# Performance work log

Measured on AMD Instinct MI355X. Metric: run time of the kernel, lower is better.

## Reference

```python
import jax, jax.numpy as jnp
import numpy as np

NUM_HEADS = 8

def setup_inputs() -> dict:
    key = jax.random.key(0)
    ks = jax.random.split(key, 7)
    B, Cin, H, W = 4, 256, 56, 56
    Cout = 256
    s = 1.0 / np.sqrt(Cin)
    return {
        "x": jax.random.normal(ks[0], (B, Cin, H, W), dtype=jnp.float32),
        "wq": jax.random.normal(ks[1], (Cout, Cin), dtype=jnp.float32) * s,
        "bq": jax.random.normal(ks[2], (Cout,), dtype=jnp.float32) * s,
        "wk": jax.random.normal(ks[3], (Cout, Cin), dtype=jnp.float32) * s,
        "bk": jax.random.normal(ks[4], (Cout,), dtype=jnp.float32) * s,
        "wv": jax.random.normal(ks[5], (Cout, Cin), dtype=jnp.float32) * s,
        "bv": jax.random.normal(ks[6], (Cout,), dtype=jnp.float32) * s,
    }

def _proj(x, w, b):
    # 1x1 conv == per-pixel linear: [B,Cin,H,W] x [Cout,Cin] -> [B,Cout,H,W]
    return jnp.einsum('bchw,oc->bohw', x, w) + b[None, :, None, None]

def reference(x, wq, bq, wk, bk, wv, bv):
    B, _, H, W = x.shape
    Cout = wq.shape[0]
    hd = Cout // NUM_HEADS
    N = H * W
    # project and reshape to [B, heads, N, head_dim]
    def split_heads(t):
        return t.reshape(B, NUM_HEADS, hd, N).transpose(0, 1, 3, 2)
    q = split_heads(_proj(x, wq, bq))
    k = split_heads(_proj(x, wk, bk))
    v = split_heads(_proj(x, wv, bv))
    scores = jnp.einsum('bhnd,bhmd->bhnm', q, k) / jnp.sqrt(jnp.float32(hd))
    attn = jax.nn.softmax(scores, axis=-1)          # [B, heads, N, N]
    out = jnp.einsum('bhnm,bhmd->bhnd', attn, v)    # [B, heads, N, hd]
    out = out.transpose(0, 1, 3, 2).reshape(B, Cout, H, W)
    return out
```

## Files before the change

kernel.cpp:

```cpp
#include <hip/hip_runtime.h>
#include <math.h>


#define NB   4
#define CIN  256
#define NPIX 3136
#define NH   8
#define HD   32
#define QSC  0.25503837897544295f

typedef float          f32x4  __attribute__((ext_vector_type(4)));
typedef short          bf16x8 __attribute__((ext_vector_type(8)));
typedef unsigned int   u32x4  __attribute__((ext_vector_type(4)));
typedef unsigned int   u32x2  __attribute__((ext_vector_type(2)));
typedef unsigned short u16x4  __attribute__((ext_vector_type(4)));

static __device__ __forceinline__ unsigned short f2bf(float f) {
  union { float f; unsigned u; } v; v.f = f;
  return (unsigned short)((v.u + 0x7fffu + ((v.u >> 16) & 1u)) >> 16);
}

static __device__ __forceinline__ float fast_exp2(float x) {
#if __has_builtin(__builtin_amdgcn_exp2f)
  return __builtin_amdgcn_exp2f(x);
#else
  return exp2f(x);
#endif
}

static __device__ __forceinline__ unsigned cvt_pk_bf16(float lo, float hi) {
  unsigned r;
  asm("v_cvt_pk_bf16_f32 %0, %1, %2" : "=v"(r) : "v"(lo), "v"(hi));
  return r;
}

static __device__ __forceinline__ void gload_lds16(const void* g, void* l) {
  __builtin_amdgcn_global_load_lds(
      (__attribute__((address_space(1))) const void*)g,
      (__attribute__((address_space(3))) void*)l, 16, 0, 0);
}

static __device__ __forceinline__ bf16x8 lds_frag16(const unsigned char* p) {
  u32x4 u = *(const u32x4*)p;
  return __builtin_bit_cast(bf16x8, u);
}

__global__ __launch_bounds__(256) void k_xpose(const float* __restrict__ x,
                                               unsigned short* __restrict__ xbT) {
  __shared__ unsigned short tile[64][66];
  const int n0 = blockIdx.x * 64, c0 = blockIdx.y * 64, b = blockIdx.z;
  const int t = threadIdx.x;
  const int cl = t >> 4, nl = (t & 15) * 4;
#pragma unroll
  for (int rep = 0; rep < 4; ++rep) {
    const int c = cl + rep * 16;
    f32x4 v = *(const f32x4*)(x + ((size_t)(b * CIN + c0 + c)) * NPIX + n0 + nl);
    tile[nl + 0][c] = f2bf(v.x);
    tile[nl + 1][c] = f2bf(v.y);
    tile[nl + 2][c] = f2bf(v.z);
    tile[nl + 3][c] = f2bf(v.w);
  }
  __syncthreads();
  const int nr = t >> 2, co = (t & 3) * 16;
  unsigned pw[8];
#pragma unroll
  for (int j = 0; j < 8; ++j)
    pw[j] = (unsigned)tile[nr][co + 2 * j] | ((unsigned)tile[nr][co + 2 * j + 1] << 16);
  unsigned short* dst = xbT + ((size_t)(b * NPIX + n0 + nr)) * 256 + c0 + co;
  u32x4 lo = {pw[0], pw[1], pw[2], pw[3]};
  u32x4 hi = {pw[4], pw[5], pw[6], pw[7]};
  *(u32x4*)dst = lo;
  *(u32x4*)(dst + 8) = hi;
}

__global__ __launch_bounds__(256) void k_wconv(const float* __restrict__ wq,
                                               const float* __restrict__ wk,
                                               const float* __restrict__ wv,
                                               unsigned short* __restrict__ wb) {
  const int i = blockIdx.x * 256 + threadIdx.x;
  const int mat = i >> 16, idx = i & 65535;
  const float* w = (mat == 0) ? wq : (mat == 1 ? wk : wv);
  const float s = (mat == 0) ? QSC : 1.0f;
  wb[i] = f2bf(w[idx] * s);
}

__global__ __launch_bounds__(256) void k_proj(
    const unsigned short* __restrict__ xbT, const unsigned short* __restrict__ wb,
    const float* __restrict__ bq, const float* __restrict__ bk,
    const float* __restrict__ bv,
    unsigned short* __restrict__ qws, unsigned short* __restrict__ kws,
    unsigned short* __restrict__ vtws) {
  __shared__ alignas(16) unsigned char lds[20480];
  const int b = blockIdx.y & 3, mat = blockIdx.y >> 2;
  const int n0 = blockIdx.x * 64;
  const int t = threadIdx.x, l = t & 63, wid = t >> 6, g = l >> 4, q = l & 15;
  const unsigned short* wmat = wb + mat * (256 * 256);

  f32x4 acc[4][4] = {};

  for (int ks = 0; ks < 8; ++ks) {
#pragma unroll
    for (int r = 0; r < 4; ++r) {
      const unsigned short* src = wmat + ((wid + 4 * r) * 16 + q) * 256 + ks * 32 + g * 8;
      gload_lds16(src, lds + (r * 256 + t) * 16);
    }
    gload_lds16(xbT + ((size_t)(b * NPIX + n0 + wid * 16 + q)) * 256 + ks * 32 + g * 8,
                lds + 16384 + t * 16);
    __syncthreads();

    bf16x8 wa[4], xf[4];
#pragma unroll
    for (int r = 0; r < 4; ++r) wa[r] = lds_frag16(lds + (r * 256 + wid * 64 + l) * 16);
#pragma unroll
    for (int nt = 0; nt < 4; ++nt) xf[nt] = lds_frag16(lds + 16384 + (nt * 64 + l) * 16);
#pragma unroll
    for (int r = 0; r < 4; ++r)
#pragma unroll
      for (int nt = 0; nt < 4; ++nt)
        acc[r][nt] = __builtin_amdgcn_mfma_f32_16x16x32_bf16(wa[r], xf[nt], acc[r][nt], 0, 0, 0);
    __syncthreads();
  }

  const float* bias = (mat == 0) ? bq : (mat == 1 ? bk : bv);
  const float bsc = (mat == 0) ? QSC : 1.0f;
#pragma unroll
  for (int r = 0; r < 4; ++r) {
    const int ob = (wid + 4 * r) * 16 + g * 4;
    const int h = ob >> 5, d0 = ob & 31;
    const float b0 = bias[ob + 0] * bsc, b1 = bias[ob + 1] * bsc;
    const float b2 = bias[ob + 2] * bsc, b3 = bias[ob + 3] * bsc;
#pragma unroll
    for (int nt = 0; nt < 4; ++nt) {
      const int n = n0 + nt * 16 + q;
      f32x4 a = acc[r][nt];
      if (mat < 2) {
        unsigned short* dst = (mat == 0) ? qws : kws;
        u16x4 pk = {f2bf(a.x + b0), f2bf(a.y + b1), f2bf(a.z + b2), f2bf(a.w + b3)};
        *(u16x4*)(dst + ((size_t)((b * NH + h) * NPIX + n)) * HD + d0) = pk;
      } else {
        unsigned short* vr = vtws + ((size_t)((b * NH + h) * HD + d0)) * NPIX + n;
        vr[0] = f2bf(a.x + b0);
        vr[(size_t)NPIX] = f2bf(a.y + b1);
        vr[(size_t)2 * NPIX] = f2bf(a.z + b2);
        vr[(size_t)3 * NPIX] = f2bf(a.w + b3);
      }
    }
  }
}

__global__ __launch_bounds__(256) void k_attn(
    const unsigned short* __restrict__ qws, const unsigned short* __restrict__ kws,
    const unsigned short* __restrict__ vtws, float* __restrict__ out) {
  __shared__ alignas(16) unsigned char lds[32768];
  const int bid = blockIdx.x;
  const int xcd = bid & 7, inner = bid >> 3;
  const int qt = inner % 25;
  const int bh = 8 * (inner / 25) + xcd;
  const int q0 = qt * 128;
  const int t = threadIdx.x, l = t & 63, wid = t >> 6, g = l >> 4, q = l & 15;

  const int nA = q0 + wid * 32 + q;
  const int nB = nA + 16;
  const int rowA = (nA < NPIX) ? nA : (NPIX - 1);
  const int rowB = (nB < NPIX) ? nB : (NPIX - 1);

  u32x4 quA = *(const u32x4*)(qws + ((size_t)(bh * NPIX + rowA)) * HD + g * 8);
  u32x4 quB = *(const u32x4*)(qws + ((size_t)(bh * NPIX + rowB)) * HD + g * 8);
  const bf16x8 qfA = __builtin_bit_cast(bf16x8, quA);
  const bf16x8 qfB = __builtin_bit_cast(bf16x8, quB);
  const u32x4 onesu = {0x3F803F80u, 0x3F803F80u, 0x3F803F80u, 0x3F803F80u};
  const bf16x8 onesf = __builtin_bit_cast(bf16x8, onesu);
  const f32x4 zero4 = {0.f, 0.f, 0.f, 0.f};

  f32x4 oA0 = zero4, oA1 = zero4, oB0 = zero4, oB1 = zero4;
  f32x4 sumA = zero4, sumB = zero4;

  const unsigned short* ksrc = kws + ((size_t)(bh * NPIX + wid * 16 + q)) * HD + g * 8;
  const unsigned short* vsrc =
      vtws + ((size_t)(bh * HD + (wid >> 1) * 16 + q)) * NPIX + (wid & 1) * 32 + g * 8;

  unsigned char* const pbaseA = lds + 16384 + wid * 4096;
  unsigned char* const pbaseB = pbaseA + 2048;

  unsigned bofs = 0;
  gload_lds16(ksrc, lds + t * 16);
  gload_lds16(vsrc, lds + 4096 + t * 16);
  __syncthreads();

  for (int kt = 0; kt < 49; ++kt) {
    if (kt < 48) {
      gload_lds16(ksrc + (size_t)(kt + 1) * 64 * HD, lds + (bofs ^ 8192) + t * 16);
      gload_lds16(vsrc + (kt + 1) * 64, lds + (bofs ^ 8192) + 4096 + t * 16);
    }
    const unsigned char* kb = lds + bofs;
    const unsigned char* vb = lds + bofs + 4096;

    f32x4 sA[4], sB[4];
    __builtin_amdgcn_s_setprio(1);
#pragma unroll
    for (int jj = 0; jj < 4; ++jj) {
      bf16x8 kf = lds_frag16(kb + (jj * 64 + l) * 16);
      sA[jj] = __builtin_amdgcn_mfma_f32_16x16x32_bf16(kf, qfA, zero4, 0, 0, 0);
      sB[jj] = __builtin_amdgcn_mfma_f32_16x16x32_bf16(kf, qfB, zero4, 0, 0, 0);
    }
    __builtin_amdgcn_s_setprio(0);

    {
      unsigned pw[8];
#pragma unroll
      for (int jj = 0; jj < 4; ++jj) {
#pragma unroll
        for (int rp = 0; rp < 2; ++rp) {
          float p0 = fast_exp2(sA[jj][2 * rp + 0]);
          float p1 = fast_exp2(sA[jj][2 * rp + 1]);
          pw[jj * 2 + rp] = cvt_pk_bf16(p0, p1);
        }
      }
      u32x4 c0 = {pw[0], pw[1], pw[2], pw[3]};
      u32x4 c1 = {pw[4], pw[5], pw[6], pw[7]};
      *(u32x4*)(pbaseA + l * 16) = c0;
      *(u32x4*)(pbaseA + 1024 + l * 16) = c1;
    }
    {
      unsigned pw[8];
#pragma unroll
      for (int jj = 0; jj < 4; ++jj) {
#pragma unroll
        for (int rp = 0; rp < 2; ++rp) {
          float p0 = fast_exp2(sB[jj][2 * rp + 0]);
          float p1 = fast_exp2(sB[jj][2 * rp + 1]);
          pw[jj * 2 + rp] = cvt_pk_bf16(p0, p1);
        }
      }
      u32x4 c0 = {pw[0], pw[1], pw[2], pw[3]};
      u32x4 c1 = {pw[4], pw[5], pw[6], pw[7]};
      *(u32x4*)(pbaseB + l * 16) = c0;
      *(u32x4*)(pbaseB + 1024 + l * 16) = c1;
    }

    asm volatile("s_waitcnt lgkmcnt(0)" ::: "memory");
    __builtin_amdgcn_sched_barrier(0);

#pragma unroll
    for (int c = 0; c < 2; ++c) {
      bf16x8 v0 = lds_frag16(vb + (c * 64 + l) * 16);
      bf16x8 v1 = lds_frag16(vb + (128 + c * 64 + l) * 16);

      const unsigned char* pA = pbaseA + c * 1024 + q * 16 + (g & 2) * 4;
      u32x2 alo = *(const u32x2*)(pA + ((2 * g) & 3) * 256);
      u32x2 ahi = *(const u32x2*)(pA + ((2 * g + 1) & 3) * 256);
      u32x4 au = {alo.x, alo.y, ahi.x, ahi.y};
      bf16x8 pfA = __builtin_bit_cast(bf16x8, au);

      const unsigned char* pB = pbaseB + c * 1024 + q * 16 + (g & 2) * 4;
      u32x2 blo = *(const u32x2*)(pB + ((2 * g) & 3) * 256);
      u32x2 bhi = *(const u32x2*)(pB + ((2 * g + 1) & 3) * 256);
      u32x4 bu = {blo.x, blo.y, bhi.x, bhi.y};
      bf16x8 pfB = __builtin_bit_cast(bf16x8, bu);

      __builtin_amdgcn_s_setprio(1);
      oA0 = __builtin_amdgcn_mfma_f32_16x16x32_bf16(v0, pfA, oA0, 0, 0, 0);
      oA1 = __builtin_amdgcn_mfma_f32_16x16x32_bf16(v1, pfA, oA1, 0, 0, 0);
      sumA = __builtin_amdgcn_mfma_f32_16x16x32_bf16(onesf, pfA, sumA, 0, 0, 0);
      oB0 = __builtin_amdgcn_mfma_f32_16x16x32_bf16(v0, pfB, oB0, 0, 0, 0);
      oB1 = __builtin_amdgcn_mfma_f32_16x16x32_bf16(v1, pfB, oB1, 0, 0, 0);
      sumB = __builtin_amdgcn_mfma_f32_16x16x32_bf16(onesf, pfB, sumB, 0, 0, 0);
      __builtin_amdgcn_s_setprio(0);
    }

    __syncthreads();
    bofs ^= 8192;
  }

  if (nA < NPIX) {
    const float inv = 1.0f / sumA[0];
    float* ob = out + (size_t)(bh * HD) * NPIX + nA;
#pragma unroll
    for (int r = 0; r < 4; ++r) {
      ob[(size_t)(g * 4 + r) * NPIX] = oA0[r] * inv;
      ob[(size_t)(16 + g * 4 + r) * NPIX] = oA1[r] * inv;
    }
  }
  if (nB < NPIX) {
    const float inv = 1.0f / sumB[0];
    float* ob = out + (size_t)(bh * HD) * NPIX + nB;
#pragma unroll
    for (int r = 0; r < 4; ++r) {
      ob[(size_t)(g * 4 + r) * NPIX] = oB0[r] * inv;
      ob[(size_t)(16 + g * 4 + r) * NPIX] = oB1[r] * inv;
    }
  }
}

extern "C" void kernel_launch(void* const* d_in, const int* in_sizes, int n_in,
                              void* d_out, int out_size, void* d_ws, size_t ws_size,
                              hipStream_t stream) {
  const float* x  = (const float*)d_in[0];
  const float* wq = (const float*)d_in[1];
  const float* bq = (const float*)d_in[2];
  const float* wk = (const float*)d_in[3];
  const float* bk = (const float*)d_in[4];
  const float* wv = (const float*)d_in[5];
  const float* bv = (const float*)d_in[6];
  float* out = (float*)d_out;

  unsigned char* ws = (unsigned char*)d_ws;
  unsigned short* xbT  = (unsigned short*)(ws);
  unsigned short* wb   = (unsigned short*)(ws + 6422528);
  unsigned short* qws  = (unsigned short*)(ws + 6815744);
  unsigned short* kws  = (unsigned short*)(ws + 13238272);
  unsigned short* vtws = (unsigned short*)(ws + 19660800);

  k_xpose<<<dim3(49, 4, 4), 256, 0, stream>>>(x, xbT);
  k_wconv<<<dim3(768), 256, 0, stream>>>(wq, wk, wv, wb);
  k_proj<<<dim3(49, 12), 256, 0, stream>>>(xbT, wb, bq, bk, bv, qws, kws, vtws);
  k_attn<<<dim3(800), 256, 0, stream>>>(qws, kws, vtws, out);
}
```

Measured before the change: 115.5 us.

## Software-pipeline attention loop: PV of previous tile overlaps QK of current tile

Restructures the attention main loop so each iteration runs the P·V MFMAs for the previous key tile and then the QK^T plus exp for the current tile. The K/V staging buffers go from double to triple buffering and the P buffer is double buffered, which removes the in-loop lgkmcnt wait and sched barrier between computing P and consuming it. LDS use grows from 32KB to 56KB per block, which may lower occupancy, and the loop gains an extra iteration for prologue and epilogue.

```diff
diff --git a/kernel.cpp b/kernel.cpp
--- a/kernel.cpp
+++ b/kernel.cpp
@@ -151,7 +151,7 @@
 __global__ __launch_bounds__(256) void k_attn(
     const unsigned short* __restrict__ qws, const unsigned short* __restrict__ kws,
     const unsigned short* __restrict__ vtws, float* __restrict__ out) {
-  __shared__ alignas(16) unsigned char lds[32768];
+  __shared__ alignas(16) unsigned char lds[57344];
   const int bid = blockIdx.x;
   const int xcd = bid & 7, inner = bid >> 3;
   const int qt = inner % 25;
@@ -179,98 +179,101 @@
   const unsigned short* vsrc =
       vtws + ((size_t)(bh * HD + (wid >> 1) * 16 + q)) * NPIX + (wid & 1) * 32 + g * 8;
 
-  unsigned char* const pbaseA = lds + 16384 + wid * 4096;
-  unsigned char* const pbaseB = pbaseA + 2048;
-
-  unsigned bofs = 0;
-  gload_lds16(ksrc, lds + t * 16);
-  gload_lds16(vsrc, lds + 4096 + t * 16);
+#define STG(kt_, s_)                                                          \
+  do {                                                                        \
+    gload_lds16(ksrc + (size_t)(kt_) * 64 * HD, lds + (s_) * 8192 + t * 16);  \
+    gload_lds16(vsrc + (size_t)(kt_) * 64, lds + (s_) * 8192 + 4096 + t * 16);\
+  } while (0)
+
+  STG(0, 0);
   __syncthreads();
 
-  for (int kt = 0; kt < 49; ++kt) {
-    if (kt < 48) {
-      gload_lds16(ksrc + (size_t)(kt + 1) * 64 * HD, lds + (bofs ^ 8192) + t * 16);
-      gload_lds16(vsrc + (kt + 1) * 64, lds + (bofs ^ 8192) + 4096 + t * 16);
-    }
-    const unsigned char* kb = lds + bofs;
-    const unsigned char* vb = lds + bofs + 4096;
-
-    f32x4 sA[4], sB[4];
-    __builtin_amdgcn_s_setprio(1);
-#pragma unroll
-    for (int jj = 0; jj < 4; ++jj) {
-      bf16x8 kf = lds_frag16(kb + (jj * 64 + l) * 16);
-      sA[jj] = __builtin_amdgcn_mfma_f32_16x16x32_bf16(kf, qfA, zero4, 0, 0, 0);
-      sB[jj] = __builtin_amdgcn_mfma_f32_16x16x32_bf16(kf, qfB, zero4, 0, 0, 0);
-    }
-    __builtin_amdgcn_s_setprio(0);
-
-    {
-      unsigned pw[8];
+  for (int kt = 0; kt <= 49; ++kt) {
+    if (kt <= 47) STG(kt + 1, (kt + 1) % 3);
+
+    if (kt >= 1) {
+      const unsigned char* vb = lds + ((kt - 1) % 3) * 8192 + 4096;
+      const unsigned char* pb = lds + 24576 + ((kt - 1) & 1) * 16384 + wid * 4096;
+#pragma unroll
+      for (int c = 0; c < 2; ++c) {
+        bf16x8 v0 = lds_frag16(vb + (c * 64 + l) * 16);
+        bf16x8 v1 = lds_frag16(vb + (128 + c * 64 + l) * 16);
+
+        const unsigned char* pA = pb + c * 1024 + q * 16 + (g & 2) * 4;
+        u32x2 alo = *(const u32x2*)(pA + ((2 * g) & 3) * 256);
+        u32x2 ahi = *(const u32x2*)(pA + ((2 * g + 1) & 3) * 256);
+        u32x4 au = {alo.x, alo.y, ahi.x, ahi.y};
+        bf16x8 pfA = __builtin_bit_cast(bf16x8, au);
+
+        const unsigned char* pB = pb + 2048 + c * 1024 + q * 16 + (g & 2) * 4;
+        u32x2 blo = *(const u32x2*)(pB + ((2 * g) & 3) * 256);
+        u32x2 bhi = *(const u32x2*)(pB + ((2 * g + 1) & 3) * 256);
+        u32x4 bu = {blo.x, blo.y, bhi.x, bhi.y};
+        bf16x8 pfB = __builtin_bit_cast(bf16x8, bu);
+
+        __builtin_amdgcn_s_setprio(1);
+        oA0 = __builtin_amdgcn_mfma_f32_16x16x32_bf16(v0, pfA, oA0, 0, 0, 0);
+        oA1 = __builtin_amdgcn_mfma_f32_16x16x32_bf16(v1, pfA, oA1, 0, 0, 0);
+        sumA = __builtin_amdgcn_mfma_f32_16x16x32_bf16(onesf, pfA, sumA, 0, 0, 0);
+        oB0 = __builtin_amdgcn_mfma_f32_16x16x32_bf16(v0, pfB, oB0, 0, 0, 0);
+        oB1 = __builtin_amdgcn_mfma_f32_16x16x32_bf16(v1, pfB, oB1, 0, 0, 0);
+        sumB = __builtin_amdgcn_mfma_f32_16x16x32_bf16(onesf, pfB, sumB, 0, 0, 0);
+        __builtin_amdgcn_s_setprio(0);
+      }
+    }
+
+    if (kt <= 48) {
+      const unsigned char* kb = lds + (kt % 3) * 8192;
+      unsigned char* const pwbA = lds + 24576 + (kt & 1) * 16384 + wid * 4096;
+      unsigned char* const pwbB = pwbA + 2048;
+
+      f32x4 sA[4], sB[4];
+      __builtin_amdgcn_s_setprio(1);
 #pragma unroll
       for (int jj = 0; jj < 4; ++jj) {
-#pragma unroll
-        for (int rp = 0; rp < 2; ++rp) {
-          float p0 = fast_exp2(sA[jj][2 * rp + 0]);
-          float p1 = fast_exp2(sA[jj][2 * rp + 1]);
-          pw[jj * 2 + rp] = cvt_pk_bf16(p0, p1);
+        bf16x8 kf = lds_frag16(kb + (jj * 64 + l) * 16);
+        sA[jj] = __builtin_amdgcn_mfma_f32_16x16x32_bf16(kf, qfA, zero4, 0, 0, 0);
+        sB[jj] = __builtin_amdgcn_mfma_f32_16x16x32_bf16(kf, qfB, zero4, 0, 0, 0);
+      }
+      __builtin_amdgcn_s_setprio(0);
+
+      {
+        unsigned pw[8];
+#pragma unroll
+        for (int jj = 0; jj < 4; ++jj) {
+#pragma unroll
+          for (int rp = 0; rp < 2; ++rp) {
+            float p0 = fast_exp2(sA[jj][2 * rp + 0]);
+            float p1 = fast_exp2(sA[jj][2 * rp + 1]);
+            pw[jj * 2 + rp] = cvt_pk_bf16(p0, p1);
+          }
         }
-      }
-      u32x4 c0 = {pw[0], pw[1], pw[2], pw[3]};
-      u32x4 c1 = {pw[4], pw[5], pw[6], pw[7]};
-      *(u32x4*)(pbaseA + l * 16) = c0;
-      *(u32x4*)(pbaseA + 1024 + l * 16) = c1;
-    }
-    {
-      unsigned pw[8];
-#pragma unroll
-      for (int jj = 0; jj < 4; ++jj) {
-#pragma unroll
-        for (int rp = 0; rp < 2; ++rp) {
-          float p0 = fast_exp2(sB[jj][2 * rp + 0]);
-          float p1 = fast_exp2(sB[jj][2 * rp + 1]);
-          pw[jj * 2 + rp] = cvt_pk_bf16(p0, p1);
+        u32x4 c0 = {pw[0], pw[1], pw[2], pw[3]};
+        u32x4 c1 = {pw[4], pw[5], pw[6], pw[7]};
+        *(u32x4*)(pwbA + l * 16) = c0;
+        *(u32x4*)(pwbA + 1024 + l * 16) = c1;
+      }
+      {
+        unsigned pw[8];
+#pragma unroll
+        for (int jj = 0; jj < 4; ++jj) {
+#pragma unroll
+          for (int rp = 0; rp < 2; ++rp) {
+            float p0 = fast_exp2(sB[jj][2 * rp + 0]);
+            float p1 = fast_exp2(sB[jj][2 * rp + 1]);
+            pw[jj * 2 + rp] = cvt_pk_bf16(p0, p1);
+          }
         }
-      }
-      u32x4 c0 = {pw[0], pw[1], pw[2], pw[3]};
-      u32x4 c1 = {pw[4], pw[5], pw[6], pw[7]};
-      *(u32x4*)(pbaseB + l * 16) = c0;
-      *(u32x4*)(pbaseB + 1024 + l * 16) = c1;
-    }
-
-    asm volatile("s_waitcnt lgkmcnt(0)" ::: "memory");
-    __builtin_amdgcn_sched_barrier(0);
-
-#pragma unroll
-    for (int c = 0; c < 2; ++c) {
-      bf16x8 v0 = lds_frag16(vb + (c * 64 + l) * 16);
-      bf16x8 v1 = lds_frag16(vb + (128 + c * 64 + l) * 16);
-
-      const unsigned char* pA = pbaseA + c * 1024 + q * 16 + (g & 2) * 4;
-      u32x2 alo = *(const u32x2*)(pA + ((2 * g) & 3) * 256);
-      u32x2 ahi = *(const u32x2*)(pA + ((2 * g + 1) & 3) * 256);
-      u32x4 au = {alo.x, alo.y, ahi.x, ahi.y};
-      bf16x8 pfA = __builtin_bit_cast(bf16x8, au);
-
-      const unsigned char* pB = pbaseB + c * 1024 + q * 16 + (g & 2) * 4;
-      u32x2 blo = *(const u32x2*)(pB + ((2 * g) & 3) * 256);
-      u32x2 bhi = *(const u32x2*)(pB + ((2 * g + 1) & 3) * 256);
-      u32x4 bu = {blo.x, blo.y, bhi.x, bhi.y};
-      bf16x8 pfB = __builtin_bit_cast(bf16x8, bu);
-
-      __builtin_amdgcn_s_setprio(1);
-      oA0 = __builtin_amdgcn_mfma_f32_16x16x32_bf16(v0, pfA, oA0, 0, 0, 0);
-      oA1 = __builtin_amdgcn_mfma_f32_16x16x32_bf16(v1, pfA, oA1, 0, 0, 0);
-      sumA = __builtin_amdgcn_mfma_f32_16x16x32_bf16(onesf, pfA, sumA, 0, 0, 0);
-      oB0 = __builtin_amdgcn_mfma_f32_16x16x32_bf16(v0, pfB, oB0, 0, 0, 0);
-      oB1 = __builtin_amdgcn_mfma_f32_16x16x32_bf16(v1, pfB, oB1, 0, 0, 0);
-      sumB = __builtin_amdgcn_mfma_f32_16x16x32_bf16(onesf, pfB, sumB, 0, 0, 0);
-      __builtin_amdgcn_s_setprio(0);
+        u32x4 c0 = {pw[0], pw[1], pw[2], pw[3]};
+        u32x4 c1 = {pw[4], pw[5], pw[6], pw[7]};
+        *(u32x4*)(pwbB + l * 16) = c0;
+        *(u32x4*)(pwbB + 1024 + l * 16) = c1;
+      }
     }
 
     __syncthreads();
-    bofs ^= 8192;
-  }
+  }
+#undef STG
 
   if (nA < NPIX) {
     const float inv = 1.0f / sumA[0];
```

After: 124.6 us. +7.9%, slower.

## Shrink attention blocks to two waves and 64 queries to remove tail padding

Applied to the files above, without the earlier changes.

The attention kernel now runs 128-thread blocks covering 64 query rows each, launched as 1568 blocks. 3136 divides evenly by 64, so the bounds clamps on Q rows and output stores are removed. Each thread now stages two K and two V chunks per tile so the 64-key tile still fills. The aim is to drop the wasted padded query tile and make the work split finer, raising occupancy and balance. The cost is that each K/V tile staged in LDS is reused by fewer queries, so more global K/V traffic per output.

```diff
diff --git a/kernel.cpp b/kernel.cpp
--- a/kernel.cpp
+++ b/kernel.cpp
@@ -148,24 +148,22 @@
   }
 }
 
-__global__ __launch_bounds__(256) void k_attn(
+__global__ __launch_bounds__(128) void k_attn(
     const unsigned short* __restrict__ qws, const unsigned short* __restrict__ kws,
     const unsigned short* __restrict__ vtws, float* __restrict__ out) {
-  __shared__ alignas(16) unsigned char lds[32768];
+  __shared__ alignas(16) unsigned char lds[24576];
   const int bid = blockIdx.x;
   const int xcd = bid & 7, inner = bid >> 3;
-  const int qt = inner % 25;
-  const int bh = 8 * (inner / 25) + xcd;
-  const int q0 = qt * 128;
+  const int qt = inner % 49;
+  const int bh = (inner / 49) * 8 + xcd;
+  const int q0 = qt * 64;
   const int t = threadIdx.x, l = t & 63, wid = t >> 6, g = l >> 4, q = l & 15;
 
   const int nA = q0 + wid * 32 + q;
   const int nB = nA + 16;
-  const int rowA = (nA < NPIX) ? nA : (NPIX - 1);
-  const int rowB = (nB < NPIX) ? nB : (NPIX - 1);
-
-  u32x4 quA = *(const u32x4*)(qws + ((size_t)(bh * NPIX + rowA)) * HD + g * 8);
-  u32x4 quB = *(const u32x4*)(qws + ((size_t)(bh * NPIX + rowB)) * HD + g * 8);
+
+  u32x4 quA = *(const u32x4*)(qws + ((size_t)(bh * NPIX + nA)) * HD + g * 8);
+  u32x4 quB = *(const u32x4*)(qws + ((size_t)(bh * NPIX + nB)) * HD + g * 8);
   const bf16x8 qfA = __builtin_bit_cast(bf16x8, quA);
   const bf16x8 qfB = __builtin_bit_cast(bf16x8, quB);
   const u32x4 onesu = {0x3F803F80u, 0x3F803F80u, 0x3F803F80u, 0x3F803F80u};
@@ -175,23 +173,35 @@
   f32x4 oA0 = zero4, oA1 = zero4, oB0 = zero4, oB1 = zero4;
   f32x4 sumA = zero4, sumB = zero4;
 
-  const unsigned short* ksrc = kws + ((size_t)(bh * NPIX + wid * 16 + q)) * HD + g * 8;
-  const unsigned short* vsrc =
-      vtws + ((size_t)(bh * HD + (wid >> 1) * 16 + q)) * NPIX + (wid & 1) * 32 + g * 8;
+  const int c0 = t, c1 = t + 128;
+  const unsigned short* ks0 =
+      kws + ((size_t)(bh * NPIX + (c0 >> 6) * 16 + (c0 & 15))) * HD + ((c0 >> 4) & 3) * 8;
+  const unsigned short* ks1 =
+      kws + ((size_t)(bh * NPIX + (c1 >> 6) * 16 + (c1 & 15))) * HD + ((c1 >> 4) & 3) * 8;
+  const unsigned short* vs0 =
+      vtws + ((size_t)(bh * HD + (c0 >> 7) * 16 + (c0 & 15))) * NPIX +
+      ((c0 >> 6) & 1) * 32 + ((c0 >> 4) & 3) * 8;
+  const unsigned short* vs1 =
+      vtws + ((size_t)(bh * HD + (c1 >> 7) * 16 + (c1 & 15))) * NPIX +
+      ((c1 >> 6) & 1) * 32 + ((c1 >> 4) & 3) * 8;
 
   unsigned char* const pbaseA = lds + 16384 + wid * 4096;
   unsigned char* const pbaseB = pbaseA + 2048;
 
+#define STG(kt_, bo_)                                                       \
+  do {                                                                      \
+    gload_lds16(ks0 + (size_t)(kt_) * 64 * HD, lds + (bo_) + c0 * 16);      \
+    gload_lds16(ks1 + (size_t)(kt_) * 64 * HD, lds + (bo_) + c1 * 16);      \
+    gload_lds16(vs0 + (size_t)(kt_) * 64, lds + (bo_) + 4096 + c0 * 16);    \
+    gload_lds16(vs1 + (size_t)(kt_) * 64, lds + (bo_) + 4096 + c1 * 16);    \
+  } while (0)
+
   unsigned bofs = 0;
-  gload_lds16(ksrc, lds + t * 16);
-  gload_lds16(vsrc, lds + 4096 + t * 16);
+  STG(0, 0);
   __syncthreads();
 
   for (int kt = 0; kt < 49; ++kt) {
-    if (kt < 48) {
-      gload_lds16(ksrc + (size_t)(kt + 1) * 64 * HD, lds + (bofs ^ 8192) + t * 16);
-      gload_lds16(vsrc + (kt + 1) * 64, lds + (bofs ^ 8192) + 4096 + t * 16);
-    }
+    if (kt < 48) STG(kt + 1, bofs ^ 8192);
     const unsigned char* kb = lds + bofs;
     const unsigned char* vb = lds + bofs + 4096;
 
@@ -216,10 +226,10 @@
           pw[jj * 2 + rp] = cvt_pk_bf16(p0, p1);
         }
       }
-      u32x4 c0 = {pw[0], pw[1], pw[2], pw[3]};
-      u32x4 c1 = {pw[4], pw[5], pw[6], pw[7]};
-      *(u32x4*)(pbaseA + l * 16) = c0;
-      *(u32x4*)(pbaseA + 1024 + l * 16) = c1;
+      u32x4 cc0 = {pw[0], pw[1], pw[2], pw[3]};
+      u32x4 cc1 = {pw[4], pw[5], pw[6], pw[7]};
+      *(u32x4*)(pbaseA + l * 16) = cc0;
+      *(u32x4*)(pbaseA + 1024 + l * 16) = cc1;
     }
     {
       unsigned pw[8];
@@ -232,10 +242,10 @@
           pw[jj * 2 + rp] = cvt_pk_bf16(p0, p1);
         }
       }
-      u32x4 c0 = {pw[0], pw[1], pw[2], pw[3]};
-      u32x4 c1 = {pw[4], pw[5], pw[6], pw[7]};
-      *(u32x4*)(pbaseB + l * 16) = c0;
-      *(u32x4*)(pbaseB + 1024 + l * 16) = c1;
+      u32x4 cc0 = {pw[0], pw[1], pw[2], pw[3]};
+      u32x4 cc1 = {pw[4], pw[5], pw[6], pw[7]};
+      *(u32x4*)(pbaseB + l * 16) = cc0;
+      *(u32x4*)(pbaseB + 1024 + l * 16) = cc1;
     }
 
     asm volatile("s_waitcnt lgkmcnt(0)" ::: "memory");
@@ -271,8 +281,9 @@
     __syncthreads();
     bofs ^= 8192;
   }
-
-  if (nA < NPIX) {
+#undef STG
+
+  {
     const float inv = 1.0f / sumA[0];
     float* ob = out + (size_t)(bh * HD) * NPIX + nA;
 #pragma unroll
@@ -281,7 +292,7 @@
       ob[(size_t)(16 + g * 4 + r) * NPIX] = oA1[r] * inv;
     }
   }
-  if (nB < NPIX) {
+  {
     const float inv = 1.0f / sumB[0];
     float* ob = out + (size_t)(bh * HD) * NPIX + nB;
 #pragma unroll
@@ -314,5 +325,5 @@
   k_xpose<<<dim3(49, 4, 4), 256, 0, stream>>>(x, xbT);
   k_wconv<<<dim3(768), 256, 0, stream>>>(wq, wk, wv, wb);
   k_proj<<<dim3(49, 12), 256, 0, stream>>>(xbT, wb, bq, bk, bv, qws, kws, vtws);
-  k_attn<<<dim3(800), 256, 0, stream>>>(qws, kws, vtws, out);
-}
+  k_attn<<<dim3(1568), 128, 0, stream>>>(qws, kws, vtws, out);
+}
```

Result: slower. 126.9 us (+9.8%).
